# Kernel tuning notes

Measured on AMD Instinct MI355X. Metric: run time of the kernel, lower is better.

The kernel has to match this reference:

```python
import jax, jax.numpy as jnp
import numpy as np

T, INPUT, POP_EXC, POP_INH = 128, 2048, 2048, 512
DT = 1e-3
TAU_SYN_INV, TAU_MEM_INV = 200.0, 100.0
V_LEAK, V_TH, V_RESET = 0.0, 1.0, 0.0
RHO_RESET = 5.0            # refractory counter reset (in steps)
ALPHA = 100.0              # SuperSpike surrogate slope (used in bwd variant)
A_PRE = A_POST = 1.0
TAU_PRE_INV = TAU_POST_INV = 50.0
ETA_PLUS = ETA_MINUS = 1e-3
W_MIN, W_MAX = 0.0, 1.0


def heaviside(x):
    return (x > 0).astype(x.dtype)


def lif_refrac_step(inp, v, i, rho):
    # norse LIF feed-forward step
    v_dec = v + DT * TAU_MEM_INV * ((V_LEAK - v) + i)
    i_dec = i * (1.0 - DT * TAU_SYN_INV)
    z = heaviside(v_dec - V_TH)
    v_new = (1.0 - z) * v_dec + z * V_RESET
    i_new = i_dec + inp
    # refractory update
    refrac = heaviside(rho)                      # neurons still refractory
    v_new = (1.0 - refrac) * v_new + refrac * V_RESET
    z = (1.0 - refrac) * z
    rho_new = (1.0 - z) * jax.nn.relu(rho - refrac) + z * RHO_RESET
    return z, v_new, i_new, rho_new


def stdp_step(z_pre, z_post, w, t_pre, t_post):
    # additive STDP (norse stdp_step_linear, mu=0) with trace low-pass filters
    t_pre = t_pre + DT * TAU_PRE_INV * (-t_pre + A_PRE * z_pre)
    t_post = t_post + DT * TAU_POST_INV * (-t_post + A_POST * z_post)
    dw = ETA_PLUS * jnp.outer(z_post, t_pre) - ETA_MINUS * jnp.outer(t_post, z_pre)
    w = jnp.clip(w + dw, W_MIN, W_MAX)           # (post, pre)
    return w, t_pre, t_post


def setup_inputs() -> dict:
    key = jax.random.key(0)
    k1, k2, k3 = jax.random.split(key, 3)
    exc_currents = 2.0 * jax.random.uniform(k1, (T, INPUT), dtype=jnp.float32)
    w_exc = 0.05 * jax.random.uniform(k2, (POP_EXC, INPUT), dtype=jnp.float32)
    w_inh = 0.05 * jax.random.uniform(k3, (POP_INH, POP_EXC), dtype=jnp.float32)
    return {"exc_currents": exc_currents, "w_exc": w_exc, "w_inh": w_inh}


def reference(exc_currents, w_exc, w_inh):
    zf = jnp.zeros
    carry0 = (
        w_exc, zf(POP_EXC), zf(POP_EXC), zf(POP_EXC),   # w, v, i, rho (exc)
        zf(INPUT), zf(POP_EXC),                         # t_pre, t_post (exc)
        w_inh, zf(POP_INH), zf(POP_INH), zf(POP_INH),   # w, v, i, rho (inh)
        zf(POP_EXC), zf(POP_INH),                       # t_pre, t_post (inh)
    )

    def step(c, x):
        (we, ve, ie, re, tpe, tqe, wi, vi, ii, ri, tpi, tqi) = c
        # excitatory STDP layer: matvec input current, LIF-refrac, STDP update
        z_e, ve, ie, re = lif_refrac_step(x @ we.T, ve, ie, re)
        we, tpe, tqe = stdp_step(x, z_e, we, tpe, tqe)
        # inhibitory STDP layer driven by excitatory spikes
        z_i, vi, ii, ri = lif_refrac_step(z_e @ wi.T, vi, ii, ri)
        wi, tpi, tqi = stdp_step(z_e, z_i, wi, tpi, tqi)
        return (we, ve, ie, re, tpe, tqe, wi, vi, ii, ri, tpi, tqi), z_e

    _, spikes = jax.lax.scan(step, carry0, exc_currents)
    return spikes  # [T, POP_EXC]
```

## Files before the change

### kernel.cpp

```cpp
#include <hip/hip_runtime.h>


constexpr int T_STEPS = 128;
constexpr int N_IN    = 2048;
constexpr int N_EXC   = 2048;
constexpr int WAVES_PER_BLOCK = 4;

__global__ __launch_bounds__(256)
void tp_precompute_kernel(const float* __restrict__ x, float* __restrict__ tp_ws) {
    const int j = blockIdx.x * blockDim.x + threadIdx.x;
    float tp = 0.f;
    #pragma unroll 4
    for (int t = 0; t < T_STEPS; ++t) {
        tp = fmaf(0.05f, x[t * N_IN + j] - tp, tp);
        tp_ws[t * N_IN + j] = tp;
    }
}

template <int CTRL, int RM>
__device__ __forceinline__ float dpp_add(float x) {
    int t = __builtin_amdgcn_update_dpp(0, __builtin_bit_cast(int, x),
                                        CTRL, RM, 0xF, true);
    return x + __builtin_bit_cast(float, t);
}

__device__ __forceinline__ float wave_sum64(float x) {
    x = dpp_add<0x111, 0xF>(x);
    x = dpp_add<0x112, 0xF>(x);
    x = dpp_add<0x114, 0xF>(x);
    x = dpp_add<0x118, 0xF>(x);
    x = dpp_add<0x142, 0xA>(x);
    x = dpp_add<0x143, 0xC>(x);
    return __builtin_bit_cast(float,
        __builtin_amdgcn_readlane(__builtin_bit_cast(int, x), 63));
}

__global__ __launch_bounds__(64 * WAVES_PER_BLOCK, 2)
void snn_exc_kernel(const float* __restrict__ x,
                    const float* __restrict__ w0,
                    const float* __restrict__ tp_ws,
                    float* __restrict__ out)
{
    const int lane = threadIdx.x & 63;
    const int wid  = threadIdx.x >> 6;
    const int row  = blockIdx.x * WAVES_PER_BLOCK + wid;

    float w[32];
    {
        const float4* wrow = reinterpret_cast<const float4*>(w0 + (size_t)row * N_IN);
        #pragma unroll
        for (int m = 0; m < 8; ++m) {
            float4 t4 = wrow[m * 64 + lane];
            w[4*m+0] = t4.x; w[4*m+1] = t4.y; w[4*m+2] = t4.z; w[4*m+3] = t4.w;
        }
    }

    const float4* xbase = reinterpret_cast<const float4*>(x) + lane;
    const float4* tpb   = reinterpret_cast<const float4*>(tp_ws) + lane;

    float4 xa[8], xb[8];
    #pragma unroll
    for (int m = 0; m < 8; ++m) xa[m] = xbase[m * 64];

    float v = 0.f, syn = 0.f, rho = 0.f, tpost = 0.f;

    auto step = [&](int t, const float4 (&xc)[8], float4 (&xn)[8]) {
        const int tn = (t + 1 < T_STEPS) ? (t + 1) : (T_STEPS - 1);
        const float4* xv = xbase + (size_t)tn * (N_IN / 4);
        #pragma unroll
        for (int m = 0; m < 8; ++m) xn[m] = xv[m * 64];

        const float v_dec = fmaf(0.1f, syn - v, v);
        const bool refrac = (rho > 0.f);
        const bool spike  = (v_dec > 1.0f) && !refrac;
        v   = (spike || refrac) ? 0.f : v_dec;
        rho = spike ? 5.0f : fmaxf(rho - (refrac ? 1.f : 0.f), 0.f);
        const float zf = spike ? 1.f : 0.f;
        tpost = fmaf(0.05f, zf - tpost, tpost);
        const float c2 = 1e-3f * tpost;
        if (lane == 0) out[t * N_EXC + row] = zf;

        float a0 = 0.f, a1 = 0.f, a2 = 0.f, a3 = 0.f;
        #pragma unroll
        for (int m = 0; m < 8; ++m) {
            a0 = fmaf(xc[m].x, w[4*m+0], a0);
            a1 = fmaf(xc[m].y, w[4*m+1], a1);
            a2 = fmaf(xc[m].z, w[4*m+2], a2);
            a3 = fmaf(xc[m].w, w[4*m+3], a3);
        }

        if (spike) {
            const float4* tq4 = tpb + (size_t)t * (N_IN / 4);
            #pragma unroll
            for (int m = 0; m < 8; ++m) {
                float4 tq = tq4[m * 64];
                w[4*m+0] = fmaxf(fmaf(1e-3f, tq.x, fmaf(-c2, xc[m].x, w[4*m+0])), 0.f);
                w[4*m+1] = fmaxf(fmaf(1e-3f, tq.y, fmaf(-c2, xc[m].y, w[4*m+1])), 0.f);
                w[4*m+2] = fmaxf(fmaf(1e-3f, tq.z, fmaf(-c2, xc[m].z, w[4*m+2])), 0.f);
                w[4*m+3] = fmaxf(fmaf(1e-3f, tq.w, fmaf(-c2, xc[m].w, w[4*m+3])), 0.f);
            }
        } else {
            #pragma unroll
            for (int m = 0; m < 8; ++m) {
                w[4*m+0] = fmaxf(fmaf(-c2, xc[m].x, w[4*m+0]), 0.f);
                w[4*m+1] = fmaxf(fmaf(-c2, xc[m].y, w[4*m+1]), 0.f);
                w[4*m+2] = fmaxf(fmaf(-c2, xc[m].z, w[4*m+2]), 0.f);
                w[4*m+3] = fmaxf(fmaf(-c2, xc[m].w, w[4*m+3]), 0.f);
            }
        }

        const float inp = wave_sum64((a0 + a1) + (a2 + a3));
        syn = fmaf(0.8f, syn, inp);
    };

    for (int t = 0; t < T_STEPS; t += 2) {
        step(t,     xa, xb);
        step(t + 1, xb, xa);
    }
}

extern "C" void kernel_launch(void* const* d_in, const int* in_sizes, int n_in,
                              void* d_out, int out_size, void* d_ws, size_t ws_size,
                              hipStream_t stream) {
    const float* x  = (const float*)d_in[0];
    const float* w0 = (const float*)d_in[1];
    float* out = (float*)d_out;

    float* tp_ws = (float*)d_ws;
    tp_precompute_kernel<<<N_IN / 256, 256, 0, stream>>>(x, tp_ws);

    dim3 grid(N_EXC / WAVES_PER_BLOCK);
    dim3 block(64 * WAVES_PER_BLOCK);
    snn_exc_kernel<<<grid, block, 0, stream>>>(x, w0, tp_ws, out);
}
```

Baseline: 95.17 us.

## Split each neuron row across two waves with LDS partial-sum exchange

Each excitatory neuron's 2048-wide dot product and STDP update is now split across two waves, each holding half the weights in registers. The per-wave partial sums go through double-buffered shared memory, with a block barrier every step, and are combined at the start of the next step. The grid doubles to 1024 blocks of two neurons, which aims to raise parallelism and occupancy across the CUs. In exchange, every timestep now pays a __syncthreads, and the x stream is loaded by twice as many waves in total. The trace loads for spiking steps are also hoisted ahead of the dot product.

```diff
diff --git a/kernel.cpp b/kernel.cpp
--- a/kernel.cpp
+++ b/kernel.cpp
@@ -4,7 +4,7 @@
 constexpr int T_STEPS = 128;
 constexpr int N_IN    = 2048;
 constexpr int N_EXC   = 2048;
-constexpr int WAVES_PER_BLOCK = 4;
+constexpr int HALF    = N_IN / 2;
 
 __global__ __launch_bounds__(256)
 void tp_precompute_kernel(const float* __restrict__ x, float* __restrict__ tp_ws) {
@@ -24,51 +24,63 @@
     return x + __builtin_bit_cast(float, t);
 }
 
-__device__ __forceinline__ float wave_sum64(float x) {
+__device__ __forceinline__ float wave_sum64_to_lane63(float x) {
     x = dpp_add<0x111, 0xF>(x);
     x = dpp_add<0x112, 0xF>(x);
     x = dpp_add<0x114, 0xF>(x);
     x = dpp_add<0x118, 0xF>(x);
     x = dpp_add<0x142, 0xA>(x);
     x = dpp_add<0x143, 0xC>(x);
-    return __builtin_bit_cast(float,
-        __builtin_amdgcn_readlane(__builtin_bit_cast(int, x), 63));
+    return x;
 }
 
-__global__ __launch_bounds__(64 * WAVES_PER_BLOCK, 2)
+__global__ __launch_bounds__(256, 4)
 void snn_exc_kernel(const float* __restrict__ x,
                     const float* __restrict__ w0,
                     const float* __restrict__ tp_ws,
                     float* __restrict__ out)
 {
-    const int lane = threadIdx.x & 63;
-    const int wid  = threadIdx.x >> 6;
-    const int row  = blockIdx.x * WAVES_PER_BLOCK + wid;
+    __shared__ float part[2][2][2];
 
-    float w[32];
+    const int tid  = threadIdx.x;
+    const int lane = tid & 63;
+    const int wid  = tid >> 6;
+    const int ni   = wid >> 1;
+    const int half = wid & 1;
+    const int row  = blockIdx.x * 2 + ni;
+
+    float w[16];
     {
-        const float4* wrow = reinterpret_cast<const float4*>(w0 + (size_t)row * N_IN);
+        const float4* wrow = reinterpret_cast<const float4*>(
+            w0 + (size_t)row * N_IN + half * HALF);
         #pragma unroll
-        for (int m = 0; m < 8; ++m) {
+        for (int m = 0; m < 4; ++m) {
             float4 t4 = wrow[m * 64 + lane];
             w[4*m+0] = t4.x; w[4*m+1] = t4.y; w[4*m+2] = t4.z; w[4*m+3] = t4.w;
         }
     }
 
-    const float4* xbase = reinterpret_cast<const float4*>(x) + lane;
-    const float4* tpb   = reinterpret_cast<const float4*>(tp_ws) + lane;
+    const float4* xbase = reinterpret_cast<const float4*>(x) + half * (HALF / 4) + lane;
+    const float4* tpb   = reinterpret_cast<const float4*>(tp_ws) + half * (HALF / 4) + lane;
 
-    float4 xa[8], xb[8];
+    float4 xa[4], xb[4];
     #pragma unroll
-    for (int m = 0; m < 8; ++m) xa[m] = xbase[m * 64];
+    for (int m = 0; m < 4; ++m) xa[m] = xbase[m * 64];
+
+    if (tid < 8) reinterpret_cast<float*>(part)[tid] = 0.f;
+    __syncthreads();
 
     float v = 0.f, syn = 0.f, rho = 0.f, tpost = 0.f;
 
-    auto step = [&](int t, const float4 (&xc)[8], float4 (&xn)[8]) {
+    auto step = [&](int t, const float4 (&xc)[4], float4 (&xn)[4]) {
         const int tn = (t + 1 < T_STEPS) ? (t + 1) : (T_STEPS - 1);
         const float4* xv = xbase + (size_t)tn * (N_IN / 4);
         #pragma unroll
-        for (int m = 0; m < 8; ++m) xn[m] = xv[m * 64];
+        for (int m = 0; m < 4; ++m) xn[m] = xv[m * 64];
+
+        const float p0 = part[(t + 1) & 1][ni][0];
+        const float p1 = part[(t + 1) & 1][ni][1];
+        syn = fmaf(0.8f, syn, p0 + p1);
 
         const float v_dec = fmaf(0.1f, syn - v, v);
         const bool refrac = (rho > 0.f);
@@ -78,11 +90,18 @@
         const float zf = spike ? 1.f : 0.f;
         tpost = fmaf(0.05f, zf - tpost, tpost);
         const float c2 = 1e-3f * tpost;
-        if (lane == 0) out[t * N_EXC + row] = zf;
+        if (half == 0 && lane == 0) out[t * N_EXC + row] = zf;
+
+        float4 tq[4];
+        if (spike) {
+            const float4* tq4 = tpb + (size_t)t * (N_IN / 4);
+            #pragma unroll
+            for (int m = 0; m < 4; ++m) tq[m] = tq4[m * 64];
+        }
 
         float a0 = 0.f, a1 = 0.f, a2 = 0.f, a3 = 0.f;
         #pragma unroll
-        for (int m = 0; m < 8; ++m) {
+        for (int m = 0; m < 4; ++m) {
             a0 = fmaf(xc[m].x, w[4*m+0], a0);
             a1 = fmaf(xc[m].y, w[4*m+1], a1);
             a2 = fmaf(xc[m].z, w[4*m+2], a2);
@@ -90,18 +109,16 @@
         }
 
         if (spike) {
-            const float4* tq4 = tpb + (size_t)t * (N_IN / 4);
             #pragma unroll
-            for (int m = 0; m < 8; ++m) {
-                float4 tq = tq4[m * 64];
-                w[4*m+0] = fmaxf(fmaf(1e-3f, tq.x, fmaf(-c2, xc[m].x, w[4*m+0])), 0.f);
-                w[4*m+1] = fmaxf(fmaf(1e-3f, tq.y, fmaf(-c2, xc[m].y, w[4*m+1])), 0.f);
-                w[4*m+2] = fmaxf(fmaf(1e-3f, tq.z, fmaf(-c2, xc[m].z, w[4*m+2])), 0.f);
-                w[4*m+3] = fmaxf(fmaf(1e-3f, tq.w, fmaf(-c2, xc[m].w, w[4*m+3])), 0.f);
+            for (int m = 0; m < 4; ++m) {
+                w[4*m+0] = fmaxf(fmaf(1e-3f, tq[m].x, fmaf(-c2, xc[m].x, w[4*m+0])), 0.f);
+                w[4*m+1] = fmaxf(fmaf(1e-3f, tq[m].y, fmaf(-c2, xc[m].y, w[4*m+1])), 0.f);
+                w[4*m+2] = fmaxf(fmaf(1e-3f, tq[m].z, fmaf(-c2, xc[m].z, w[4*m+2])), 0.f);
+                w[4*m+3] = fmaxf(fmaf(1e-3f, tq[m].w, fmaf(-c2, xc[m].w, w[4*m+3])), 0.f);
             }
         } else {
             #pragma unroll
-            for (int m = 0; m < 8; ++m) {
+            for (int m = 0; m < 4; ++m) {
                 w[4*m+0] = fmaxf(fmaf(-c2, xc[m].x, w[4*m+0]), 0.f);
                 w[4*m+1] = fmaxf(fmaf(-c2, xc[m].y, w[4*m+1]), 0.f);
                 w[4*m+2] = fmaxf(fmaf(-c2, xc[m].z, w[4*m+2]), 0.f);
@@ -109,8 +126,9 @@
             }
         }
 
-        const float inp = wave_sum64((a0 + a1) + (a2 + a3));
-        syn = fmaf(0.8f, syn, inp);
+        const float s = wave_sum64_to_lane63((a0 + a1) + (a2 + a3));
+        if (lane == 63) part[t & 1][ni][half] = s;
+        __syncthreads();
     };
 
     for (int t = 0; t < T_STEPS; t += 2) {
@@ -129,7 +147,7 @@
     float* tp_ws = (float*)d_ws;
     tp_precompute_kernel<<<N_IN / 256, 256, 0, stream>>>(x, tp_ws);
 
-    dim3 grid(N_EXC / WAVES_PER_BLOCK);
-    dim3 block(64 * WAVES_PER_BLOCK);
+    dim3 grid(N_EXC / 2);
+    dim3 block(256);
     snn_exc_kernel<<<grid, block, 0, stream>>>(x, w0, tp_ws, out);
 }
```

New measurement: 102.5 us. 1.08x slower.
